# Performance work log

Measured on AMD Instinct MI355X. Metric: run time of the kernel, lower is better.

## Reference

```python
import jax, jax.numpy as jnp
import numpy as np

B, S, IN_DIM, D_MODEL, H = 8, 1024, 512, 1024, 16
DEPTH = D_MODEL // H
LN_EPS = 1e-5


def setup_inputs() -> dict:
    key = jax.random.key(0)
    ks = jax.random.split(key, 10)
    def xavier(k, shape):
        fan_in, fan_out = shape[0], shape[1]
        lim = float(np.sqrt(6.0 / (fan_in + fan_out)))
        return jax.random.uniform(k, shape, jnp.float32, -lim, lim)
    return {
        "x": jax.random.normal(ks[0], (B, S, IN_DIM), jnp.float32),
        "mask": jax.random.randint(ks[1], (H, S, S), 0, 2, jnp.int32),
        "wq_w": xavier(ks[2], (IN_DIM, D_MODEL)),
        "wq_b": jnp.zeros((D_MODEL,), jnp.float32),
        "wk_w": xavier(ks[3], (IN_DIM, D_MODEL)),
        "wk_b": jnp.zeros((D_MODEL,), jnp.float32),
        "wv_w": xavier(ks[4], (IN_DIM, D_MODEL)),
        "wv_b": jnp.zeros((D_MODEL,), jnp.float32),
        "dense_w": xavier(ks[5], (D_MODEL, D_MODEL)),
        "dense_b": jnp.zeros((D_MODEL,), jnp.float32),
        "res_w": xavier(ks[6], (IN_DIM, D_MODEL)),  # residual_linear (no bias)
        "ln_g": 1.0 + 0.02 * jax.random.normal(ks[7], (D_MODEL,), jnp.float32),
        "ln_b": 0.02 * jax.random.normal(ks[8], (D_MODEL,), jnp.float32),
    }


def reference(x, mask, wq_w, wq_b, wk_w, wk_b, wv_w, wv_b,
              dense_w, dense_b, res_w, ln_g, ln_b):
    bs = x.shape[0]
    residual = x @ res_w  # [B,S,D_MODEL]
    # project and split heads -> [B,H,S,depth]
    def split(t):
        return t.reshape(bs, -1, H, DEPTH).transpose(0, 2, 1, 3)
    q = split(x @ wq_w + wq_b)
    k = split(x @ wk_w + wk_b)
    v = split(x @ wv_w + wv_b)
    scale = 1.0 / jnp.sqrt(jnp.asarray(DEPTH, x.dtype))
    attn = jnp.einsum("bhqd,bhkd->bhqk", q, k) * scale
    attn = jnp.where(mask[None] == 0, jnp.asarray(-1e9, attn.dtype), attn)
    attn = jax.nn.softmax(attn, axis=-1)  # dropout is identity in eval
    out = jnp.einsum("bhqk,bhkd->bhqd", attn, v)
    out = out.transpose(0, 2, 1, 3).reshape(bs, -1, D_MODEL)
    out = out @ dense_w + dense_b
    # residual + LayerNorm
    y = residual + out
    mu = jnp.mean(y, axis=-1, keepdims=True)
    var = jnp.mean(jnp.square(y - mu), axis=-1, keepdims=True)
    y = (y - mu) * jax.lax.rsqrt(var + LN_EPS)
    return y * ln_g + ln_b
```

## Files before the change

### kernel.cpp

```cpp
#include <hip/hip_runtime.h>
#include <stdint.h>

#define B_ 8
#define S_ 1024
#define IN_DIM 512
#define DM 1024
#define H_ 16
#define DEP 64

typedef __bf16 bf16;
typedef __attribute__((ext_vector_type(8))) __bf16 bf16x8;
typedef __attribute__((ext_vector_type(4))) __bf16 bf16x4;
typedef __attribute__((ext_vector_type(4))) short short4v;
typedef __attribute__((ext_vector_type(4))) float f32x4;

#if defined(__has_builtin)
#if __has_builtin(__builtin_amdgcn_mfma_f32_16x16x16_bf16)
#define HAVE_NEW16 1
#endif
#endif
static __device__ __forceinline__ f32x4 mfma16(bf16x4 a, bf16x4 b, f32x4 c) {
#ifdef HAVE_NEW16
    return __builtin_amdgcn_mfma_f32_16x16x16_bf16(a, b, c, 0, 0, 0);
#else
    union { bf16x4 h; short4v s; } ua, ub;
    ua.h = a; ub.h = b;
    return __builtin_amdgcn_mfma_f32_16x16x16bf16_1k(ua.s, ub.s, c, 0, 0, 0);
#endif
}

static __device__ __forceinline__ void gld_lds16(const void* g, void* l) {
    __builtin_amdgcn_global_load_lds(
        (const __attribute__((address_space(1))) uint32_t*)g,
        (__attribute__((address_space(3))) uint32_t*)l, 16, 0, 0);
}

static __device__ __forceinline__ float ldin(const void* p, size_t i, int isb) {
    return isb ? (float)((const bf16*)p)[i] : ((const float*)p)[i];
}

static __device__ __forceinline__ int ldsch(int r, int q4) {
    const int pr = r >> 1;
    return pr*8 + ((((r & 1) << 2) + q4) ^ (pr & 7));
}

__global__ __launch_bounds__(256) void prep_kernel(
    const uint16_t* __restrict__ xraw, const void* __restrict__ x,
    const void* __restrict__ wq, const void* __restrict__ wk, const void* __restrict__ wv,
    const void* __restrict__ res, const void* __restrict__ dense,
    const int* __restrict__ mask,
    bf16* __restrict__ wqT, bf16* __restrict__ wkT, bf16* __restrict__ wvT,
    bf16* __restrict__ resT, bf16* __restrict__ denseT,
    const void* b0, const void* b1, const void* b2, const void* b3,
    const void* b4, const void* b5, bf16* __restrict__ small,
    bf16* __restrict__ xc, unsigned long long* __restrict__ mb, int* __restrict__ flag)
{
    __shared__ int s_isb;
    __shared__ bf16 tile[32][33];
    const int tid = threadIdx.x;

    if (tid < 64) {
        int sane = 0;
        #pragma unroll
        for (int j = 0; j < 8; j++) {
            const uint16_t u = xraw[tid * 8 + j];
            const int e = (u >> 7) & 0xff;
            sane += ((u & 0x7fff) == 0 || (e >= 100 && e <= 140)) ? 1 : 0;
        }
        #pragma unroll
        for (int m = 1; m < 64; m <<= 1) sane += __shfl_xor(sane, m);
        if (tid == 0) s_isb = (sane >= 450) ? 1 : 0;
    }
    __syncthreads();
    const int isb = s_isb;
    const int bid = blockIdx.x;
    if (bid == 0 && tid == 0) *flag = isb;

    if (bid < 1024) {
        const int w = tid >> 6, lane = tid & 63;
        const int gw = bid * 4 + w;
        for (int c = gw; c < 262144; c += 4096) {
            const int v = mask[(size_t)c * 64 + lane];
            const unsigned long long bits = __ballot(v != 0);
            if (lane == 0) mb[c] = bits;
        }
    } else if (bid < 5120) {
        const size_t i = ((size_t)(bid - 1024) * 256 + tid) * 4;
        if (isb) {
            *(bf16x4*)(xc + i) = *(const bf16x4*)((const bf16*)x + i);
        } else {
            const float4 v = *(const float4*)((const float*)x + i);
            bf16x4 o; o[0] = (bf16)v.x; o[1] = (bf16)v.y; o[2] = (bf16)v.z; o[3] = (bf16)v.w;
            *(bf16x4*)(xc + i) = o;
        }
    } else if (bid < 8192) {
        const int t = bid - 5120;
        const int z = t >> 9, rem = t & 511;
        const void* src; bf16* dst; int kb, kd;
        if (z == 0)      { src = wq;    dst = wqT;    kb = 0;   kd = 512;  }
        else if (z == 1) { src = wk;    dst = wkT;    kb = 0;   kd = 512;  }
        else if (z == 2) { src = wv;    dst = wvT;    kb = 0;   kd = 512;  }
        else if (z == 3) { src = res;   dst = resT;   kb = 0;   kd = 512;  }
        else if (z == 4) { src = dense; dst = denseT; kb = 0;   kd = 1024; }
        else             { src = dense; dst = denseT; kb = 512; kd = 1024; }
        const int n0 = (rem & 31) * 32, k0 = (rem >> 5) * 32;
        const int tx = tid & 31, ty = tid >> 5;
        #pragma unroll
        for (int r = 0; r < 4; r++)
            tile[ty + r*8][tx] = (bf16)ldin(src, (size_t)(kb + k0 + ty + r*8) * DM + n0 + tx, isb);
        __syncthreads();
        #pragma unroll
        for (int r = 0; r < 4; r++)
            dst[(size_t)(n0 + ty + r*8) * kd + kb + k0 + tx] = tile[tx][ty + r*8];
    } else {
        const int s6 = bid - 8192;
        const void* srcs[6] = {b0, b1, b2, b3, b4, b5};
        const void* s = srcs[s6];
        for (int i = tid; i < 1024; i += 256)
            small[s6 * 1024 + i] = (bf16)ldin(s, i, isb);
    }
}

template<int KDIM>
static __device__ __forceinline__ void gemm_core(
    const bf16* __restrict__ A, const bf16* __restrict__ BT,
    int m0, int n0, bf16* Asm, bf16* Bsm, f32x4 acc[4][4])
{
    const int tid = threadIdx.x, l = tid & 63, w = tid >> 6;
    const int wm = w >> 1, wn = w & 1, quad = l >> 4, l15 = l & 15;
    #pragma unroll
    for (int i = 0; i < 4; i++)
        #pragma unroll
        for (int j = 0; j < 4; j++) acc[i][j] = f32x4{0.f, 0.f, 0.f, 0.f};

    constexpr int NIT = KDIM / 32;
    const int lp  = l >> 3;
    const int s0  = (l & 7) ^ lp;
    const int rof = s0 >> 2;
    const int kch = (s0 & 3) * 8;

    #pragma unroll
    for (int qq = 0; qq < 2; qq++) {
        const int row = (qq*32 + w*8 + lp)*2 + rof;
        gld_lds16(A  + (size_t)(m0 + row)*KDIM + kch, Asm + (qq*256 + w*64)*8);
        gld_lds16(BT + (size_t)(n0 + row)*KDIM + kch, Bsm + (qq*256 + w*64)*8);
    }

    for (int it = 0; it < NIT; it++) {
        __syncthreads();
        const int cur = (it & 1) * 4096;
        const int nxt = cur ^ 4096;
        if (it + 1 < NIT) {
            const int k1 = (it + 1) * 32;
            #pragma unroll
            for (int qq = 0; qq < 2; qq++) {
                const int row = (qq*32 + w*8 + lp)*2 + rof;
                gld_lds16(A  + (size_t)(m0 + row)*KDIM + k1 + kch, Asm + nxt + (qq*256 + w*64)*8);
                gld_lds16(BT + (size_t)(n0 + row)*KDIM + k1 + kch, Bsm + nxt + (qq*256 + w*64)*8);
            }
        }
        bf16x8 af[4], bfv[4];
        #pragma unroll
        for (int i = 0; i < 4; i++)
            af[i] = *(const bf16x8*)(Asm + cur + ldsch(wm*64 + i*16 + l15, quad)*8);
        #pragma unroll
        for (int j = 0; j < 4; j++)
            bfv[j] = *(const bf16x8*)(Bsm + cur + ldsch(wn*64 + j*16 + l15, quad)*8);
        #pragma unroll
        for (int i = 0; i < 4; i++)
            #pragma unroll
            for (int j = 0; j < 4; j++)
                acc[i][j] = __builtin_amdgcn_mfma_f32_16x16x32_bf16(af[i], bfv[j], acc[i][j], 0, 0, 0);
    }
}

#define EPI_P 132
__global__ __launch_bounds__(256) void proj_kernel(
    const bf16* __restrict__ x,
    const bf16* __restrict__ wqT, const bf16* __restrict__ wkT,
    const bf16* __restrict__ wvT, const bf16* __restrict__ resT,
    const bf16* __restrict__ small,
    bf16* __restrict__ Q, bf16* __restrict__ K, bf16* __restrict__ VtG, bf16* __restrict__ R)
{
    __shared__ alignas(16) char smem[32768];
    bf16* Asm = (bf16*)smem;
    bf16* Bsm = (bf16*)(smem + 16384);
    bf16* epi = (bf16*)smem;

    const int m0 = blockIdx.x * 128;
    const int ng = blockIdx.y * 128;
    const int sel = ng >> 10, n0 = ng & 1023;
    const bf16* BT; const bf16* bias = nullptr;
    if (sel == 0)      { BT = wqT; bias = small;        }
    else if (sel == 1) { BT = wkT; bias = small + 1024; }
    else if (sel == 2) { BT = wvT; bias = small + 2048; }
    else               { BT = resT; }

    f32x4 acc[4][4];
    gemm_core<IN_DIM>(x, BT, m0, n0, Asm, Bsm, acc);

    const int tid = threadIdx.x, l = tid & 63, w = tid >> 6;
    const int wm = w >> 1, wn = w & 1, quad = l >> 4, l15 = l & 15;

    if (sel == 2) {
        const int bb = m0 >> 10, srow0 = m0 & 1023;
        #pragma unroll
        for (int hf = 0; hf < 2; hf++) {
            __syncthreads();
            if (wn == hf) {
                #pragma unroll
                for (int j = 0; j < 4; j++) {
                    const int cl = j*16 + l15;
                    const float bv = (float)bias[n0 + hf*64 + cl];
                    #pragma unroll
                    for (int i = 0; i < 4; i++) {
                        const int rho = wm*64 + i*16 + quad*4;
                        #pragma unroll
                        for (int r = 0; r < 4; r++)
                            epi[cl*EPI_P + rho + r] = (bf16)(acc[i][j][r] + bv);
                    }
                }
            }
            __syncthreads();
            const int hh = (n0 >> 6) + hf;
            const int sc = tid & 15;
            #pragma unroll
            for (int pass = 0; pass < 4; pass++) {
                const int dl = (tid >> 4) + pass*16;
                bf16x8 v;
                #pragma unroll
                for (int k = 0; k < 8; k++) {
                    const int pl = (sc & 3)*8 + k;
                    const int kl = ((pl & 4) << 2) | ((pl & 24) >> 1) | (pl & 3);
                    v[k] = epi[dl*EPI_P + (sc >> 2)*32 + kl];
                }
                *(bf16x8*)(VtG + ((size_t)(bb*16 + hh)*64 + dl)*S_ + srow0 + sc*8) = v;
            }
        }
        return;
    }

    #pragma unroll
    for (int j = 0; j < 4; j++) {
        const int col = n0 + wn*64 + j*16 + l15;
        const float bv = (sel < 3) ? (float)bias[col] : 0.f;
        #pragma unroll
        for (int i = 0; i < 4; i++) {
            const int rb = m0 + wm*64 + i*16 + quad*4;
            #pragma unroll
            for (int r = 0; r < 4; r++) {
                const float v = acc[i][j][r] + bv;
                if (sel == 0)      Q[(size_t)(rb + r)*DM + col] = (bf16)(v * 0.18033688f);
                else if (sel == 1) K[(size_t)(rb + r)*DM + col] = (bf16)v;
                else               R[(size_t)(rb + r)*DM + col] = (bf16)v;
            }
        }
    }
}

__global__ __launch_bounds__(256) void attn_kernel(
    const bf16* __restrict__ Q, const bf16* __restrict__ K, const bf16* __restrict__ VtG,
    const unsigned long long* __restrict__ mb, bf16* __restrict__ AO)
{
    __shared__ alignas(16) bf16 Ksm[2*64*64];
    __shared__ alignas(16) bf16 Vsm[2*64*64];

    const int tid = threadIdx.x, l = tid & 63, w = tid >> 6;
    const int quad = l >> 4, l15 = l & 15;

    const int fid = blockIdx.y * 8 + blockIdx.x;
    const int xcd = fid & 7, idx = fid >> 3;
    const int bh  = xcd * 16 + (idx >> 3);
    const int qt  = idx & 7;
    const int b = bh >> 4, h = bh & 15;
    const int wrow = qt*128 + w*32;
    const size_t rowbase = (size_t)b * S_;

    bf16x8 qa[2][2];
    #pragma unroll
    for (int g = 0; g < 2; g++) {
        const bf16* qp = Q + (rowbase + wrow + g*16 + l15)*DM + h*DEP + quad*8;
        qa[g][0] = *(const bf16x8*)qp;
        qa[g][1] = *(const bf16x8*)(qp + 32);
    }
    const bf16* kgbase = K + rowbase*DM + h*DEP;
    const bf16* vgbase = VtG + (size_t)(b*16 + h)*64*S_;
    const unsigned long long* mbase[2];
    #pragma unroll
    for (int g = 0; g < 2; g++)
        mbase[g] = mb + ((size_t)h*S_ + wrow + g*16 + l15) * 16;

    uint32_t bmr[4];
    #pragma unroll
    for (int r = 0; r < 4; r++) bmr[r] = 1u << (quad*4 + r);

    bf16x4 onesv;
    #pragma unroll
    for (int r = 0; r < 4; r++) onesv[r] = (bf16)1.0f;

    f32x4 oT[2][4];
    f32x4 lacc[2];
    #pragma unroll
    for (int g = 0; g < 2; g++) {
        lacc[g] = f32x4{0.f,0.f,0.f,0.f};
        #pragma unroll
        for (int dt = 0; dt < 4; dt++) oT[g][dt] = f32x4{0.f,0.f,0.f,0.f};
    }

    const int srow8 = l >> 3;
    const int gch   = (l & 7) ^ srow8;

    #pragma unroll
    for (int q = 0; q < 2; q++) {
        const int row = q*32 + w*8 + srow8;
        gld_lds16(kgbase + (size_t)row*DM + gch*8, Ksm + (q*256 + w*64)*8);
        gld_lds16(vgbase + (size_t)row*S_ + gch*8, Vsm + (q*256 + w*64)*8);
    }
    uint32_t mlo[2], mhi[2];
    #pragma unroll
    for (int g = 0; g < 2; g++) {
        const unsigned long long mw = mbase[g][0];
        mlo[g] = (uint32_t)mw; mhi[g] = (uint32_t)(mw >> 32);
    }

    const int rsw = l15 & 7;

    for (int it = 0; it < 16; it++) {
        __syncthreads();
        const int cur = (it & 1) * 4096, nxt = cur ^ 4096;
        const bf16* Kc = Ksm + cur;
        const bf16* Vc = Vsm + cur;

        const uint32_t cmlo[2] = {mlo[0], mlo[1]}, cmhi[2] = {mhi[0], mhi[1]};
        if (it + 1 < 16) {
            #pragma unroll
            for (int q = 0; q < 2; q++) {
                const int row = q*32 + w*8 + srow8;
                gld_lds16(kgbase + (size_t)((it+1)*64 + row)*DM + gch*8,
                          Ksm + nxt + (q*256 + w*64)*8);
                gld_lds16(vgbase + (size_t)row*S_ + (it+1)*64 + gch*8,
                          Vsm + nxt + (q*256 + w*64)*8);
            }
            #pragma unroll
            for (int g = 0; g < 2; g++) {
                const unsigned long long mw = mbase[g][it + 1];
                mlo[g] = (uint32_t)mw; mhi[g] = (uint32_t)(mw >> 32);
            }
        }

        #pragma unroll
        for (int sub = 0; sub < 2; sub++) {
            bf16x8 kf[2][2];
            bf16x8 va8[4];
            #pragma unroll
            for (int h2 = 0; h2 < 2; h2++) {
                const int krow = sub*32 + h2*16 + l15;
                kf[h2][0] = *(const bf16x8*)(Kc + krow*64 + ((quad    ) ^ rsw)*8);
                kf[h2][1] = *(const bf16x8*)(Kc + krow*64 + ((quad + 4) ^ rsw)*8);
            }
            #pragma unroll
            for (int dt = 0; dt < 4; dt++)
                va8[dt] = *(const bf16x8*)(Vc + (dt*16 + l15)*64 + ((sub*4 + quad) ^ rsw)*8);

            #pragma unroll
            for (int g = 0; g < 2; g++) {
                f32x4 st[2];
                __builtin_amdgcn_s_setprio(1);
                #pragma unroll
                for (int h2 = 0; h2 < 2; h2++) {
                    f32x4 z = {0.f,0.f,0.f,0.f};
                    z = __builtin_amdgcn_mfma_f32_16x16x32_bf16(kf[h2][0], qa[g][0], z, 0, 0, 0);
                    z = __builtin_amdgcn_mfma_f32_16x16x32_bf16(kf[h2][1], qa[g][1], z, 0, 0, 0);
                    st[h2] = z;
                }
                __builtin_amdgcn_s_setprio(0);
                const uint32_t msk = sub ? cmhi[g] : cmlo[g];
                bf16x4 pb[2];
                #pragma unroll
                for (int h2 = 0; h2 < 2; h2++) {
                    const uint32_t mh = msk >> (h2 * 16);
                    #pragma unroll
                    for (int r = 0; r < 4; r++) {
                        const float e = __builtin_amdgcn_exp2f(st[h2][r]);
                        const float pv = (mh & bmr[r]) ? e : 0.f;
                        pb[h2][r] = (bf16)pv;
                    }
                }
                __builtin_amdgcn_s_setprio(1);
                #pragma unroll
                for (int h2 = 0; h2 < 2; h2++) {
                    lacc[g] = mfma16(onesv, pb[h2], lacc[g]);
                    #pragma unroll
                    for (int dt = 0; dt < 4; dt++) {
                        const bf16x4 vh = h2
                            ? __builtin_shufflevector(va8[dt], va8[dt], 4, 5, 6, 7)
                            : __builtin_shufflevector(va8[dt], va8[dt], 0, 1, 2, 3);
                        oT[g][dt] = mfma16(vh, pb[h2], oT[g][dt]);
                    }
                }
                __builtin_amdgcn_s_setprio(0);
            }
        }
    }

    #pragma unroll
    for (int g = 0; g < 2; g++) {
        const float inv = 1.0f / lacc[g][0];
        bf16* aor = AO + (rowbase + wrow + g*16 + l15)*DM + h*DEP;
        #pragma unroll
        for (int dt = 0; dt < 4; dt++) {
            bf16x4 ov;
            #pragma unroll
            for (int r = 0; r < 4; r++) ov[r] = (bf16)(oT[g][dt][r] * inv);
            *(bf16x4*)(aor + dt*16 + quad*4) = ov;
        }
    }
}

__global__ __launch_bounds__(256) void dense_kernel(
    const bf16* __restrict__ AOin, const bf16* __restrict__ dT,
    const bf16* __restrict__ db, bf16* __restrict__ R)
{
    __shared__ alignas(16) bf16 Asm[2*64*32];
    __shared__ alignas(16) bf16 Bsm[2*128*32];
    const int m0 = blockIdx.x * 64, n0 = blockIdx.y * 128;
    const int tid = threadIdx.x, l = tid & 63, w = tid >> 6;
    const int wm = w >> 1, wn = w & 1, quad = l >> 4, l15 = l & 15;

    f32x4 acc[2][4];
    #pragma unroll
    for (int i = 0; i < 2; i++)
        #pragma unroll
        for (int j = 0; j < 4; j++) acc[i][j] = f32x4{0.f, 0.f, 0.f, 0.f};

    const int lp  = l >> 3;
    const int s0  = (l & 7) ^ lp;
    const int rof = s0 >> 2;
    const int kch = (s0 & 3) * 8;

    gld_lds16(AOin + (size_t)(m0 + (w*8 + lp)*2 + rof)*DM + kch, Asm + (w*64)*8);
    #pragma unroll
    for (int qq = 0; qq < 2; qq++) {
        const int row = (qq*32 + w*8 + lp)*2 + rof;
        gld_lds16(dT + (size_t)(n0 + row)*DM + kch, Bsm + (qq*256 + w*64)*8);
    }

    for (int it = 0; it < 32; it++) {
        __syncthreads();
        const int curA = (it & 1) * 2048, nxtA = curA ^ 2048;
        const int curB = (it & 1) * 4096, nxtB = curB ^ 4096;
        if (it + 1 < 32) {
            const int k1 = (it + 1) * 32;
            gld_lds16(AOin + (size_t)(m0 + (w*8 + lp)*2 + rof)*DM + k1 + kch, Asm + nxtA + (w*64)*8);
            #pragma unroll
            for (int qq = 0; qq < 2; qq++) {
                const int row = (qq*32 + w*8 + lp)*2 + rof;
                gld_lds16(dT + (size_t)(n0 + row)*DM + k1 + kch, Bsm + nxtB + (qq*256 + w*64)*8);
            }
        }
        bf16x8 af[2], bfv[4];
        #pragma unroll
        for (int i = 0; i < 2; i++)
            af[i] = *(const bf16x8*)(Asm + curA + ldsch(wm*32 + i*16 + l15, quad)*8);
        #pragma unroll
        for (int j = 0; j < 4; j++)
            bfv[j] = *(const bf16x8*)(Bsm + curB + ldsch(wn*64 + j*16 + l15, quad)*8);
        #pragma unroll
        for (int i = 0; i < 2; i++)
            #pragma unroll
            for (int j = 0; j < 4; j++)
                acc[i][j] = __builtin_amdgcn_mfma_f32_16x16x32_bf16(af[i], bfv[j], acc[i][j], 0, 0, 0);
    }

    #pragma unroll
    for (int j = 0; j < 4; j++) {
        const int col = n0 + wn*64 + j*16 + l15;
        const float bv = (float)db[col];
        #pragma unroll
        for (int i = 0; i < 2; i++) {
            const int rb = m0 + wm*32 + i*16 + quad*4;
            #pragma unroll
            for (int r = 0; r < 4; r++) {
                const size_t idx = (size_t)(rb + r)*DM + col;
                R[idx] = (bf16)((float)R[idx] + acc[i][j][r] + bv);
            }
        }
    }
}

__global__ __launch_bounds__(256) void ln_kernel(
    const bf16* __restrict__ R, const bf16* __restrict__ small,
    void* __restrict__ out, const int* __restrict__ flag)
{
    const int isb = *flag;
    const int row  = blockIdx.x * 4 + (threadIdx.x >> 6);
    const int lane = threadIdx.x & 63;
    const bf16* rp = R + (size_t)row*DM;

    float v[16];
    float s = 0.f;
    #pragma unroll
    for (int k = 0; k < 4; k++) {
        const bf16x4 rv = *(const bf16x4*)(rp + k*256 + lane*4);
        #pragma unroll
        for (int r = 0; r < 4; r++) { v[k*4+r] = (float)rv[r]; s += v[k*4+r]; }
    }
    #pragma unroll
    for (int m = 1; m < 64; m <<= 1) s += __shfl_xor(s, m);
    const float mu = s * (1.0f/DM);

    float q = 0.f;
    #pragma unroll
    for (int i = 0; i < 16; i++) { v[i] -= mu; q += v[i]*v[i]; }
    #pragma unroll
    for (int m = 1; m < 64; m <<= 1) q += __shfl_xor(q, m);
    const float rstd = rsqrtf(q * (1.0f/DM) + 1e-5f);

    #pragma unroll
    for (int k = 0; k < 4; k++) {
        const int col = k*256 + lane*4;
        const bf16x4 gv = *(const bf16x4*)(small + 4*1024 + col);
        const bf16x4 bv = *(const bf16x4*)(small + 5*1024 + col);
        float o[4];
        #pragma unroll
        for (int r = 0; r < 4; r++) o[r] = v[k*4+r]*rstd*(float)gv[r] + (float)bv[r];
        if (isb) {
            bf16x4 ov;
            #pragma unroll
            for (int r = 0; r < 4; r++) ov[r] = (bf16)o[r];
            *(bf16x4*)((bf16*)out + (size_t)row*DM + col) = ov;
        } else {
            float4 ov = {o[0], o[1], o[2], o[3]};
            *(float4*)((float*)out + (size_t)row*DM + col) = ov;
        }
    }
}

extern "C" void kernel_launch(void* const* d_in, const int* in_sizes, int n_in,
                              void* d_out, int out_size, void* d_ws, size_t ws_size,
                              hipStream_t stream) {
    const int* mask = (const int*)d_in[1];

    char* ws = (char*)d_ws;
    bf16* wqT   = (bf16*)(ws);
    bf16* wkT   = (bf16*)(ws + ((size_t)1 << 20));
    bf16* wvT   = (bf16*)(ws + ((size_t)2 << 20));
    bf16* resT  = (bf16*)(ws + ((size_t)3 << 20));
    bf16* dT    = (bf16*)(ws + ((size_t)4 << 20));
    bf16* small = (bf16*)(ws + ((size_t)6 << 20));
    int*  flag  = (int*) (ws + ((size_t)6 << 20) + 16384);
    unsigned long long* mbits = (unsigned long long*)(ws + ((size_t)7 << 20));
    bf16* Qb    = (bf16*)(ws + ((size_t)9  << 20));
    bf16* Kb    = (bf16*)(ws + ((size_t)25 << 20));
    bf16* VtG   = (bf16*)(ws + ((size_t)41 << 20));
    bf16* R     = (bf16*)(ws + ((size_t)57 << 20));
    bf16* xc    = (bf16*)d_out;

    prep_kernel<<<8198, 256, 0, stream>>>(
        (const uint16_t*)d_in[0], d_in[0],
        d_in[2], d_in[4], d_in[6], d_in[10], d_in[8],
        mask,
        wqT, wkT, wvT, resT, dT,
        d_in[3], d_in[5], d_in[7], d_in[9], d_in[11], d_in[12], small,
        xc, mbits, flag);
    proj_kernel<<<dim3(64, 32), 256, 0, stream>>>(
        xc, wqT, wkT, wvT, resT, small, Qb, Kb, VtG, R);
    attn_kernel<<<dim3(8, 128), 256, 0, stream>>>(Qb, Kb, VtG, mbits, Qb );
    dense_kernel<<<dim3(128, 8), 256, 0, stream>>>(Qb, dT, small + 3*1024, R);
    ln_kernel<<<2048, 256, 0, stream>>>(R, small, d_out, flag);
}
```

Before: 332.4 us.

## Triple-buffer GEMM LDS staging with partial vmcnt waits in proj and dense kernels

Changes the K-loop in the projection GEMM core and the dense kernel from double buffering to triple buffering. Loads are issued two stages ahead, and each stage boundary uses an explicit s_waitcnt on vmcnt with a partial count plus s_barrier instead of __syncthreads. The goal is to keep global-to-LDS loads in flight across iterations and hide memory latency behind the MFMA work. In exchange LDS use per block rises (48KB in proj), which may lower occupancy, and correctness depends on the hand-written vmcnt counts matching the number of loads each stage issues.

```diff
diff --git a/kernel.cpp b/kernel.cpp
--- a/kernel.cpp
+++ b/kernel.cpp
@@ -37,6 +37,13 @@
 
 static __device__ __forceinline__ float ldin(const void* p, size_t i, int isb) {
     return isb ? (float)((const bf16*)p)[i] : ((const float*)p)[i];
+}
+
+template<int N>
+static __device__ __forceinline__ void wait_barrier() {
+    if constexpr (N == 4)      asm volatile("s_waitcnt vmcnt(4) lgkmcnt(0)\ns_barrier" ::: "memory");
+    else if constexpr (N == 3) asm volatile("s_waitcnt vmcnt(3) lgkmcnt(0)\ns_barrier" ::: "memory");
+    else                       asm volatile("s_waitcnt vmcnt(0) lgkmcnt(0)\ns_barrier" ::: "memory");
 }
 
 static __device__ __forceinline__ int ldsch(int r, int q4) {
@@ -139,26 +146,24 @@
     const int rof = s0 >> 2;
     const int kch = (s0 & 3) * 8;
 
-    #pragma unroll
-    for (int qq = 0; qq < 2; qq++) {
-        const int row = (qq*32 + w*8 + lp)*2 + rof;
-        gld_lds16(A  + (size_t)(m0 + row)*KDIM + kch, Asm + (qq*256 + w*64)*8);
-        gld_lds16(BT + (size_t)(n0 + row)*KDIM + kch, Bsm + (qq*256 + w*64)*8);
-    }
-
-    for (int it = 0; it < NIT; it++) {
-        __syncthreads();
-        const int cur = (it & 1) * 4096;
-        const int nxt = cur ^ 4096;
-        if (it + 1 < NIT) {
-            const int k1 = (it + 1) * 32;
-            #pragma unroll
-            for (int qq = 0; qq < 2; qq++) {
-                const int row = (qq*32 + w*8 + lp)*2 + rof;
-                gld_lds16(A  + (size_t)(m0 + row)*KDIM + k1 + kch, Asm + nxt + (qq*256 + w*64)*8);
-                gld_lds16(BT + (size_t)(n0 + row)*KDIM + k1 + kch, Bsm + nxt + (qq*256 + w*64)*8);
-            }
-        }
+    auto stage = [&](int t, int bo) {
+        const int k0 = t * 32;
+        #pragma unroll
+        for (int qq = 0; qq < 2; qq++) {
+            const int row = (qq*32 + w*8 + lp)*2 + rof;
+            gld_lds16(A  + (size_t)(m0 + row)*KDIM + k0 + kch, Asm + bo + (qq*256 + w*64)*8);
+            gld_lds16(BT + (size_t)(n0 + row)*KDIM + k0 + kch, Bsm + bo + (qq*256 + w*64)*8);
+        }
+    };
+
+    stage(0, 0);
+    stage(1, 4096);
+    int cur = 0;
+    for (int it = 0; it < NIT; ++it) {
+        if (it < NIT - 1) wait_barrier<4>();
+        else              wait_barrier<0>();
+        if (it + 2 < NIT)
+            stage(it + 2, (cur >= 4096) ? cur - 4096 : cur + 8192);
         bf16x8 af[4], bfv[4];
         #pragma unroll
         for (int i = 0; i < 4; i++)
@@ -171,6 +176,7 @@
             #pragma unroll
             for (int j = 0; j < 4; j++)
                 acc[i][j] = __builtin_amdgcn_mfma_f32_16x16x32_bf16(af[i], bfv[j], acc[i][j], 0, 0, 0);
+        cur = (cur == 8192) ? 0 : cur + 4096;
     }
 }
 
@@ -182,9 +188,9 @@
     const bf16* __restrict__ small,
     bf16* __restrict__ Q, bf16* __restrict__ K, bf16* __restrict__ VtG, bf16* __restrict__ R)
 {
-    __shared__ alignas(16) char smem[32768];
+    __shared__ alignas(16) char smem[49152];
     bf16* Asm = (bf16*)smem;
-    bf16* Bsm = (bf16*)(smem + 16384);
+    bf16* Bsm = (bf16*)(smem + 24576);
     bf16* epi = (bf16*)smem;
 
     const int m0 = blockIdx.x * 128;
@@ -421,8 +427,8 @@
     const bf16* __restrict__ AOin, const bf16* __restrict__ dT,
     const bf16* __restrict__ db, bf16* __restrict__ R)
 {
-    __shared__ alignas(16) bf16 Asm[2*64*32];
-    __shared__ alignas(16) bf16 Bsm[2*128*32];
+    __shared__ alignas(16) bf16 Asm[3*64*32];
+    __shared__ alignas(16) bf16 Bsm[3*128*32];
     const int m0 = blockIdx.x * 64, n0 = blockIdx.y * 128;
     const int tid = threadIdx.x, l = tid & 63, w = tid >> 6;
     const int wm = w >> 1, wn = w & 1, quad = l >> 4, l15 = l & 15;
@@ -438,26 +444,25 @@
     const int rof = s0 >> 2;
     const int kch = (s0 & 3) * 8;
 
-    gld_lds16(AOin + (size_t)(m0 + (w*8 + lp)*2 + rof)*DM + kch, Asm + (w*64)*8);
-    #pragma unroll
-    for (int qq = 0; qq < 2; qq++) {
-        const int row = (qq*32 + w*8 + lp)*2 + rof;
-        gld_lds16(dT + (size_t)(n0 + row)*DM + kch, Bsm + (qq*256 + w*64)*8);
-    }
-
-    for (int it = 0; it < 32; it++) {
-        __syncthreads();
-        const int curA = (it & 1) * 2048, nxtA = curA ^ 2048;
-        const int curB = (it & 1) * 4096, nxtB = curB ^ 4096;
-        if (it + 1 < 32) {
-            const int k1 = (it + 1) * 32;
-            gld_lds16(AOin + (size_t)(m0 + (w*8 + lp)*2 + rof)*DM + k1 + kch, Asm + nxtA + (w*64)*8);
-            #pragma unroll
-            for (int qq = 0; qq < 2; qq++) {
-                const int row = (qq*32 + w*8 + lp)*2 + rof;
-                gld_lds16(dT + (size_t)(n0 + row)*DM + k1 + kch, Bsm + nxtB + (qq*256 + w*64)*8);
-            }
-        }
+    auto stage = [&](int t, int boA, int boB) {
+        const int k1 = t * 32;
+        gld_lds16(AOin + (size_t)(m0 + (w*8 + lp)*2 + rof)*DM + k1 + kch, Asm + boA + (w*64)*8);
+        #pragma unroll
+        for (int qq = 0; qq < 2; qq++) {
+            const int row = (qq*32 + w*8 + lp)*2 + rof;
+            gld_lds16(dT + (size_t)(n0 + row)*DM + k1 + kch, Bsm + boB + (qq*256 + w*64)*8);
+        }
+    };
+
+    stage(0, 0, 0);
+    stage(1, 2048, 4096);
+    int curA = 0, curB = 0;
+    for (int it = 0; it < 32; ++it) {
+        if (it < 31) wait_barrier<3>();
+        else         wait_barrier<0>();
+        if (it + 2 < 32)
+            stage(it + 2, (curA >= 2048) ? curA - 2048 : curA + 4096,
+                          (curB >= 4096) ? curB - 4096 : curB + 8192);
         bf16x8 af[2], bfv[4];
         #pragma unroll
         for (int i = 0; i < 2; i++)
@@ -470,6 +475,8 @@
             #pragma unroll
             for (int j = 0; j < 4; j++)
                 acc[i][j] = __builtin_amdgcn_mfma_f32_16x16x32_bf16(af[i], bfv[j], acc[i][j], 0, 0, 0);
+        curA = (curA == 4096) ? 0 : curA + 2048;
+        curB = (curB == 8192) ? 0 : curB + 4096;
     }
 
     #pragma unroll
```

After: 322.0 us. -3.1%, faster.
